# Kernel tuning notes

Measured on AMD Instinct MI355X. Metric: run time of the kernel, lower is better.

The kernel has to match this reference:

```python
import jax, jax.numpy as jnp
import numpy as np

BS = 8192
INPUT_DIM = 4096
LAYER_DIMS = [64, 256, 64]
BLOCK_DIM = LAYER_DIMS[0]
N_BLOCKS = INPUT_DIM // BLOCK_DIM


def setup_inputs() -> dict:
    key = jax.random.key(0)
    kx, kw1, kw2 = jax.random.split(key, 3)
    x = jax.random.normal(kx, (BS, INPUT_DIM), dtype=jnp.float32)
    # BlockLinear params: weight ~ randn, bias ~ zeros (as in torch source)
    W1 = jax.random.normal(kw1, (N_BLOCKS, LAYER_DIMS[0], LAYER_DIMS[1]), dtype=jnp.float32)
    b1 = jnp.zeros((N_BLOCKS, 1, LAYER_DIMS[1]), dtype=jnp.float32)
    W2 = jax.random.normal(kw2, (N_BLOCKS, LAYER_DIMS[1], LAYER_DIMS[2]), dtype=jnp.float32)
    b2 = jnp.zeros((N_BLOCKS, 1, LAYER_DIMS[2]), dtype=jnp.float32)
    return {"x": x, "W1": W1, "b1": b1, "W2": W2, "b2": b2}


def reference(x, W1, b1, W2, b2):
    bs = x.shape[0]
    # [bs, input_dim] -> [n_blocks, bs, block_dim]
    h = x.reshape(bs, N_BLOCKS, BLOCK_DIM).transpose(1, 0, 2)
    # BlockLinear 1 (bmm + bias) then exact GELU (torch nn.GELU default)
    h = jnp.einsum('nbi,nio->nbo', h, W1) + b1
    h = jax.nn.gelu(h, approximate=False)
    # BlockLinear 2
    h = jnp.einsum('nbi,nio->nbo', h, W2) + b2
    # [n_blocks, bs, out_block] -> [bs, n_blocks*out_block]
    return h.transpose(1, 0, 2).reshape(bs, -1)
```

## Files before the change

kernel.cpp:

```cpp
#include <hip/hip_runtime.h>

using f16x8 = _Float16 __attribute__((ext_vector_type(8)));
using f32x4 = float __attribute__((ext_vector_type(4)));

#define BS      8192
#define IN_DIM  4096
#define NB      64
#define BD      64
#define HID     256
#define OD      64
#define GY      32

__device__ __forceinline__ float gelu_f(float z) {
    float t = z * z;
    float p = __builtin_fmaf(0.044715f * z, t, z);
    float e = __builtin_amdgcn_exp2f(p * 2.3021193f);
    float r = __builtin_amdgcn_rcpf(e + 1.0f);
    return __builtin_fmaf(-z, r, z);
}

__global__ __launch_bounds__(512, 4) void blockmlp_kernel(
    const float* __restrict__ xg, const float* __restrict__ w1g,
    const float* __restrict__ b1g, const float* __restrict__ w2g,
    const float* __restrict__ b2g, float* __restrict__ outg) {

    __shared__ _Float16 W1F[2048 * 8];
    __shared__ _Float16 W2L[2048 * 8];
    __shared__ float    b1L[HID];

    const int tid = threadIdx.x;
    const int w   = tid >> 6;
    const int l   = tid & 63;
    const int g   = l >> 4;
    const int l15 = l & 15;
    const int n   = blockIdx.x;

    const float* W1n = w1g + (size_t)n * (BD * HID);
    #pragma unroll
    for (int i4 = 0; i4 < 4; ++i4) {
        int e  = i4 * 512 + tid;
        int ht = e >> 7;
        int ks = (e >> 6) & 1;
        int le = e & 63;
        int ge = le >> 4, oo = le & 15;
        f16x8 v;
        #pragma unroll
        for (int j = 0; j < 8; ++j)
            v[j] = (_Float16)W1n[(size_t)(ks * 32 + ge * 8 + j) * HID + ht * 16 + oo];
        *(f16x8*)&W1F[e * 8] = v;
    }

    const float* W2n = w2g + (size_t)n * (HID * OD);
    #pragma unroll
    for (int i4 = 0; i4 < 4; ++i4) {
        int e  = i4 * 512 + tid;
        int p  = e >> 8;
        int n2 = (e >> 6) & 3;
        int le = e & 63;
        int ge = le >> 4, ce = le & 15;
        f16x8 v;
        #pragma unroll
        for (int j = 0; j < 8; ++j)
            v[j] = (_Float16)W2n[(size_t)(p * 32 + ((j >> 2) << 4) + ge * 4 + (j & 3)) * OD + n2 * 16 + ce];
        *(f16x8*)&W2L[e * 8] = v;
    }

    if (tid < HID) b1L[tid] = b1g[n * HID + tid];

    float b2b[4];
    #pragma unroll
    for (int n2 = 0; n2 < 4; ++n2) b2b[n2] = b2g[n * OD + n2 * 16 + l15];

    __syncthreads();

    const int row0 = blockIdx.y * 256 + w * 32;

    f16x8 xa[2][2];
    #pragma unroll
    for (int rs = 0; rs < 2; ++rs)
        #pragma unroll
        for (int ks = 0; ks < 2; ++ks) {
            const float* px = xg + (size_t)(row0 + rs * 16 + l15) * IN_DIM + n * BD + ks * 32 + g * 8;
            float4 lo = *(const float4*)px;
            float4 hi = *(const float4*)(px + 4);
            f16x8 v;
            v[0] = (_Float16)lo.x; v[1] = (_Float16)lo.y;
            v[2] = (_Float16)lo.z; v[3] = (_Float16)lo.w;
            v[4] = (_Float16)hi.x; v[5] = (_Float16)hi.y;
            v[6] = (_Float16)hi.z; v[7] = (_Float16)hi.w;
            xa[rs][ks] = v;
        }

    const f32x4 z4 = {0.0f, 0.0f, 0.0f, 0.0f};
    f32x4 c2[2][4];
    #pragma unroll
    for (int rs = 0; rs < 2; ++rs)
        #pragma unroll
        for (int n2 = 0; n2 < 4; ++n2) c2[rs][n2] = z4;

    #pragma unroll
    for (int p = 0; p < 8; ++p) {
        f32x4 c1[2][2];
        #pragma unroll
        for (int htl = 0; htl < 2; ++htl) {
            f32x4 ca = z4, cb = z4;
            #pragma unroll
            for (int ks = 0; ks < 2; ++ks) {
                f16x8 wf = *(const f16x8*)&W1F[((((p * 2 + htl) * 2) + ks) * 64 + l) * 8];
                ca = __builtin_amdgcn_mfma_f32_16x16x32_f16(wf, xa[0][ks], ca, 0, 0, 0);
                cb = __builtin_amdgcn_mfma_f32_16x16x32_f16(wf, xa[1][ks], cb, 0, 0, 0);
            }
            c1[htl][0] = ca; c1[htl][1] = cb;
        }
        f32x4 b1a = *(const f32x4*)&b1L[(p * 2 + 0) * 16 + g * 4];
        f32x4 b1b = *(const f32x4*)&b1L[(p * 2 + 1) * 16 + g * 4];
        f16x8 a2[2];
        #pragma unroll
        for (int rs = 0; rs < 2; ++rs) {
            f16x8 v;
            #pragma unroll
            for (int q = 0; q < 4; ++q) {
                v[q]     = (_Float16)gelu_f(c1[0][rs][q] + b1a[q]);
                v[q + 4] = (_Float16)gelu_f(c1[1][rs][q] + b1b[q]);
            }
            a2[rs] = v;
        }
        #pragma unroll
        for (int n2 = 0; n2 < 4; ++n2) {
            f16x8 bf = *(const f16x8*)&W2L[((p * 4 + n2) * 64 + l) * 8];
            c2[0][n2] = __builtin_amdgcn_mfma_f32_16x16x32_f16(a2[0], bf, c2[0][n2], 0, 0, 0);
            c2[1][n2] = __builtin_amdgcn_mfma_f32_16x16x32_f16(a2[1], bf, c2[1][n2], 0, 0, 0);
        }
    }

    #pragma unroll
    for (int rs = 0; rs < 2; ++rs)
        #pragma unroll
        for (int n2 = 0; n2 < 4; ++n2)
            #pragma unroll
            for (int q = 0; q < 4; ++q) {
                int row = row0 + rs * 16 + g * 4 + q;
                outg[(size_t)row * IN_DIM + n * BD + n2 * 16 + l15] = c2[rs][n2][q] + b2b[n2];
            }
}

extern "C" void kernel_launch(void* const* d_in, const int* in_sizes, int n_in,
                              void* d_out, int out_size, void* d_ws, size_t ws_size,
                              hipStream_t stream) {
    const float* x  = (const float*)d_in[0];
    const float* W1 = (const float*)d_in[1];
    const float* b1 = (const float*)d_in[2];
    const float* W2 = (const float*)d_in[3];
    const float* b2 = (const float*)d_in[4];
    float* out = (float*)d_out;

    dim3 grid(NB, GY, 1);
    dim3 block(512, 1, 1);
    hipLaunchKernelGGL(blockmlp_kernel, grid, block, 0, stream, x, W1, b1, W2, b2, out);
}
```

Baseline: 78.42 us.

## Pre-pack fp16 MFMA weight tiles in a separate kernel before the main MLP

```diff
diff --git a/kernel.cpp b/kernel.cpp
--- a/kernel.cpp
+++ b/kernel.cpp
@@ -19,14 +19,46 @@
     return __builtin_fmaf(-z, r, z);
 }
 
+__global__ __launch_bounds__(256) void prep_weights(
+    const float* __restrict__ w1g, const float* __restrict__ w2g,
+    f16x8* __restrict__ ws1, f16x8* __restrict__ ws2) {
+    const int n = blockIdx.x;
+    const int t = threadIdx.x;
+    const float* W1n = w1g + (size_t)n * (BD * HID);
+    const float* W2n = w2g + (size_t)n * (HID * OD);
+    #pragma unroll
+    for (int it = 0; it < 8; ++it) {
+        int e = it * 256 + t;
+        {
+            int ht = e >> 7, ks = (e >> 6) & 1, le = e & 63;
+            int ge = le >> 4, oo = le & 15;
+            f16x8 v;
+            #pragma unroll
+            for (int j = 0; j < 8; ++j)
+                v[j] = (_Float16)W1n[(size_t)(ks * 32 + ge * 8 + j) * HID + ht * 16 + oo];
+            ws1[(size_t)n * 2048 + e] = v;
+        }
+        {
+            int p = e >> 8, n2 = (e >> 6) & 3, le = e & 63;
+            int ge = le >> 4, ce = le & 15;
+            f16x8 v;
+            #pragma unroll
+            for (int j = 0; j < 8; ++j)
+                v[j] = (_Float16)W2n[(size_t)(p * 32 + ((j >> 2) << 4) + ge * 4 + (j & 3)) * OD + n2 * 16 + ce];
+            ws2[(size_t)n * 2048 + e] = v;
+        }
+    }
+}
+
 __global__ __launch_bounds__(512, 4) void blockmlp_kernel(
-    const float* __restrict__ xg, const float* __restrict__ w1g,
-    const float* __restrict__ b1g, const float* __restrict__ w2g,
-    const float* __restrict__ b2g, float* __restrict__ outg) {
+    const float* __restrict__ xg,
+    const f16x8* __restrict__ ws1, const f16x8* __restrict__ ws2,
+    const float* __restrict__ b1g, const float* __restrict__ b2g,
+    float* __restrict__ outg) {
 
-    __shared__ _Float16 W1F[2048 * 8];
-    __shared__ _Float16 W2L[2048 * 8];
-    __shared__ float    b1L[HID];
+    __shared__ f16x8 W1F[2048];
+    __shared__ f16x8 W2L[2048];
+    __shared__ float b1L[HID];
 
     const int tid = threadIdx.x;
     const int w   = tid >> 6;
@@ -35,35 +67,17 @@
     const int l15 = l & 15;
     const int n   = blockIdx.x;
 
-    const float* W1n = w1g + (size_t)n * (BD * HID);
+    const f16x8* p1 = ws1 + (size_t)n * 2048;
+    const f16x8* p2 = ws2 + (size_t)n * 2048;
+    f16x8 s1[4], s2[4];
     #pragma unroll
-    for (int i4 = 0; i4 < 4; ++i4) {
-        int e  = i4 * 512 + tid;
-        int ht = e >> 7;
-        int ks = (e >> 6) & 1;
-        int le = e & 63;
-        int ge = le >> 4, oo = le & 15;
-        f16x8 v;
-        #pragma unroll
-        for (int j = 0; j < 8; ++j)
-            v[j] = (_Float16)W1n[(size_t)(ks * 32 + ge * 8 + j) * HID + ht * 16 + oo];
-        *(f16x8*)&W1F[e * 8] = v;
-    }
-
-    const float* W2n = w2g + (size_t)n * (HID * OD);
+    for (int it = 0; it < 4; ++it) { s1[it] = p1[it * 512 + tid]; }
     #pragma unroll
-    for (int i4 = 0; i4 < 4; ++i4) {
-        int e  = i4 * 512 + tid;
-        int p  = e >> 8;
-        int n2 = (e >> 6) & 3;
-        int le = e & 63;
-        int ge = le >> 4, ce = le & 15;
-        f16x8 v;
-        #pragma unroll
-        for (int j = 0; j < 8; ++j)
-            v[j] = (_Float16)W2n[(size_t)(p * 32 + ((j >> 2) << 4) + ge * 4 + (j & 3)) * OD + n2 * 16 + ce];
-        *(f16x8*)&W2L[e * 8] = v;
-    }
+    for (int it = 0; it < 4; ++it) { s2[it] = p2[it * 512 + tid]; }
+    #pragma unroll
+    for (int it = 0; it < 4; ++it) { W1F[it * 512 + tid] = s1[it]; }
+    #pragma unroll
+    for (int it = 0; it < 4; ++it) { W2L[it * 512 + tid] = s2[it]; }
 
     if (tid < HID) b1L[tid] = b1g[n * HID + tid];
 
@@ -106,7 +120,7 @@
             f32x4 ca = z4, cb = z4;
             #pragma unroll
             for (int ks = 0; ks < 2; ++ks) {
-                f16x8 wf = *(const f16x8*)&W1F[((((p * 2 + htl) * 2) + ks) * 64 + l) * 8];
+                f16x8 wf = W1F[(((p * 2 + htl) * 2) + ks) * 64 + l];
                 ca = __builtin_amdgcn_mfma_f32_16x16x32_f16(wf, xa[0][ks], ca, 0, 0, 0);
                 cb = __builtin_amdgcn_mfma_f32_16x16x32_f16(wf, xa[1][ks], cb, 0, 0, 0);
             }
@@ -127,7 +141,7 @@
         }
         #pragma unroll
         for (int n2 = 0; n2 < 4; ++n2) {
-            f16x8 bf = *(const f16x8*)&W2L[((p * 4 + n2) * 64 + l) * 8];
+            f16x8 bf = W2L[(p * 4 + n2) * 64 + l];
             c2[0][n2] = __builtin_amdgcn_mfma_f32_16x16x32_f16(a2[0], bf, c2[0][n2], 0, 0, 0);
             c2[1][n2] = __builtin_amdgcn_mfma_f32_16x16x32_f16(a2[1], bf, c2[1][n2], 0, 0, 0);
         }
@@ -154,7 +168,10 @@
     const float* b2 = (const float*)d_in[4];
     float* out = (float*)d_out;
 
-    dim3 grid(NB, GY, 1);
-    dim3 block(512, 1, 1);
-    hipLaunchKernelGGL(blockmlp_kernel, grid, block, 0, stream, x, W1, b1, W2, b2, out);
+    f16x8* ws1 = (f16x8*)d_ws;
+    f16x8* ws2 = ws1 + (size_t)NB * 2048;
+
+    hipLaunchKernelGGL(prep_weights, dim3(NB), dim3(256), 0, stream, W1, W2, ws1, ws2);
+    hipLaunchKernelGGL(blockmlp_kernel, dim3(NB, GY), dim3(512), 0, stream,
+                       x, ws1, ws2, b1, b2, out);
 }
```

After: 77.65 us. About the same (-1.0%).
